# Optimization experiments

Measured on AMD Instinct MI355X. Metric: run time of the kernel, lower is better.

## Reference

```python
import jax, jax.numpy as jnp
import numpy as np

B, D, L = 2, 1024, 4096   # batch, channels (= num_heads), seq len
FS = 4                    # filter_size
DEPTH = 11                # ceil(log2((L-1)/(FS-1)+1))
LN_EPS = 1e-5


def setup_inputs() -> dict:
    key = jax.random.key(0)
    ks = jax.random.split(key, 7)
    return {
        "x": jax.random.normal(ks[0], (B, D, L), jnp.float32),
        "h0": jax.random.normal(ks[1], (D, 1, FS), jnp.float32) * 0.2,
        "h1": jax.random.normal(ks[2], (D, 1, FS), jnp.float32) * 0.2,
        "w_mix": jax.random.normal(ks[3], (D, D), jnp.float32) / np.sqrt(D),
        "b_mix": jnp.zeros((D,), jnp.float32),
        "ln_gamma": jnp.ones((D,), jnp.float32),
        "ln_beta": jnp.zeros((D,), jnp.float32),
    }


def _dw_conv(a, h, dilation):
    # depthwise (groups = D) dilated conv1d, cross-correlation like torch
    return jax.lax.conv_general_dilated(
        a, h, window_strides=(1,), padding='VALID',
        rhs_dilation=(dilation,),
        dimension_numbers=('NCH', 'OIH', 'NCH'),
        feature_group_count=D)


def reference(x, h0, h1, w_mix, b_mix, ln_gamma, ln_beta):
    # --- multires conv tree ---
    a = x
    dilation = 1
    a_list, b_list = [], []
    for _ in range(DEPTH):
        pad = dilation * (FS - 1)
        ap = jnp.pad(a, ((0, 0), (0, 0), (pad, 0)))  # left causal pad
        b = _dw_conv(ap, h1, dilation)
        a = _dw_conv(ap, h0, dilation)
        a_list.append(a)
        b_list.append(b)
        dilation *= 2
    # --- gated combination across scales (deepest level first) ---
    a_rev = a_list[::-1]
    b_rev = b_list[::-1]
    y = jnp.zeros_like(x)
    gated = None
    for i in range(DEPTH):
        if i + 1 < DEPTH:
            gated = jax.nn.sigmoid(a_rev[i]) * b_rev[i + 1]
        # last iteration reuses the previous gated tensor (matches original)
        y = y + gated
    # --- 1x1 channel mix (Dropout1d is identity in eval) + residual ---
    mixed = jnp.einsum('oc,bcl->bol', w_mix, y) + b_mix[None, :, None]
    z = mixed + x
    # --- LayerNorm over channel dim ---
    mu = jnp.mean(z, axis=1, keepdims=True)
    var = jnp.mean(jnp.square(z - mu), axis=1, keepdims=True)
    out = (z - mu) * jax.lax.rsqrt(var + LN_EPS)
    out = out * ln_gamma[None, :, None] + ln_beta[None, :, None]
    return out
```

## Files before the change

### kernel.cpp

```cpp
#include <hip/hip_runtime.h>
#include <hip/hip_bf16.h>

#define NB 2
#define ND 1024
#define NL 4096
#define NFS 4
#define NDEPTH 11
#define LN_EPS 1e-5f

#define BM 128
#define BN 128
#define BK 32

#define CPAD 384

typedef __bf16 bf16x8 __attribute__((ext_vector_type(8)));
typedef float f32x4 __attribute__((ext_vector_type(4)));

__device__ __forceinline__ unsigned short f2bf(float f) {
    __hip_bfloat16 h = __float2bfloat16(f);
    unsigned short u;
    __builtin_memcpy(&u, &h, 2);
    return u;
}

__device__ __forceinline__ float bf2f(unsigned short u) {
    unsigned int ui = (unsigned int)u << 16;
    float f;
    __builtin_memcpy(&f, &ui, 4);
    return f;
}

__device__ __forceinline__ unsigned int pack2bf(float lo, float hi) {
    return (unsigned int)f2bf(lo) | ((unsigned int)f2bf(hi) << 16);
}

__device__ __forceinline__ float sigm(float v) {
    return __builtin_amdgcn_rcpf(1.f + __expf(-v));
}

__device__ __forceinline__ void llds16(const void* g, void* l) {
    __builtin_amdgcn_global_load_lds(
        (const __attribute__((address_space(1))) unsigned int*)g,
        (__attribute__((address_space(3))) unsigned int*)l, 16, 0, 0);
}

__global__ __launch_bounds__(256) void wconv_kernel(const float* __restrict__ w,
                                                    unsigned short* __restrict__ wbf) {
    const int idx8 = (blockIdx.x * 256 + threadIdx.x) * 8;
    const float4 v0 = *reinterpret_cast<const float4*>(w + idx8);
    const float4 v1 = *reinterpret_cast<const float4*>(w + idx8 + 4);
    uint4 o;
    o.x = pack2bf(v0.x, v0.y);
    o.y = pack2bf(v0.z, v0.w);
    o.z = pack2bf(v1.x, v1.y);
    o.w = pack2bf(v1.z, v1.w);
    *reinterpret_cast<uint4*>(wbf + idx8) = o;
}

__global__ __launch_bounds__(256) void conv_cascade_kernel(const float* __restrict__ x,
                                                           const float* __restrict__ h0,
                                                           const float* __restrict__ h1,
                                                           unsigned short* __restrict__ ybf) {
    __shared__ float a_sh[CPAD + NL];
    const int row = blockIdx.x;
    const int d = row & (ND - 1);
    const int t = threadIdx.x;

    if (t < CPAD - 256) a_sh[t] = 0.f;
    a_sh[(CPAD - 256) + t] = 0.f;

    const float* xrow = x + (size_t)row * NL;

    float h0c[NFS], h1c[NFS];
#pragma unroll
    for (int k = 0; k < NFS; ++k) {
        h0c[k] = h0[d * NFS + k];
        h1c[k] = h1[d * NFS + k];
    }

    float cur[16], yacc[16], bprev[16];
#pragma unroll
    for (int i = 0; i < 16; ++i) {
        cur[i] = xrow[i * 256 + t];
        a_sh[CPAD + i * 256 + t] = cur[i];
        yacc[i] = 0.f;
        bprev[i] = 0.f;
    }
    __syncthreads();

    int dil = 1;
#pragma unroll 1
    for (int lev = 0; lev < 7; ++lev) {
        const int off1 = CPAD + t - dil;
        const int off2 = CPAD + t - 2 * dil;
        const int off3 = CPAD + t - 3 * dil;
        float anew[16], bnew[16];
#pragma unroll
        for (int i = 0; i < 16; ++i) {
            const float a0 = cur[i];
            const float a1 = a_sh[off1 + i * 256];
            const float a2 = a_sh[off2 + i * 256];
            const float a3 = a_sh[off3 + i * 256];
            anew[i] = h0c[3] * a0 + h0c[2] * a1 + h0c[1] * a2 + h0c[0] * a3;
            bnew[i] = h1c[3] * a0 + h1c[2] * a1 + h1c[1] * a2 + h1c[0] * a3;
        }
        __syncthreads();
#pragma unroll
        for (int i = 0; i < 16; ++i) a_sh[CPAD + i * 256 + t] = anew[i];

        if (lev >= 1) {
            const float sc = (lev == 1) ? 2.f : 1.f;
#pragma unroll
            for (int i = 0; i < 16; ++i)
                yacc[i] += sc * sigm(anew[i]) * bprev[i];
        }
#pragma unroll
        for (int i = 0; i < 16; ++i) {
            cur[i] = anew[i];
            bprev[i] = bnew[i];
        }
        dil <<= 1;
        __syncthreads();
    }

    {
        const int off1 = CPAD + t - 128;
        const int off2 = CPAD + t - 256;
        const int off3 = CPAD + t - 384;
        float anew[16], bnew[16];
#pragma unroll
        for (int i = 0; i < 16; ++i) {
            const float a0 = cur[i];
            const float a1 = a_sh[off1 + i * 256];
            const float a2 = a_sh[off2 + i * 256];
            const float a3 = a_sh[off3 + i * 256];
            anew[i] = h0c[3] * a0 + h0c[2] * a1 + h0c[1] * a2 + h0c[0] * a3;
            bnew[i] = h1c[3] * a0 + h1c[2] * a1 + h1c[1] * a2 + h1c[0] * a3;
        }
#pragma unroll
        for (int i = 0; i < 16; ++i) {
            yacc[i] += sigm(anew[i]) * bprev[i];
            cur[i] = anew[i];
            bprev[i] = bnew[i];
        }
    }

    {
        float anew[16], bnew[16];
#pragma unroll
        for (int i = 0; i < 16; ++i) {
            const float a0 = cur[i];
            const float a1 = (i >= 1) ? cur[i - 1] : 0.f;
            const float a2 = (i >= 2) ? cur[i - 2] : 0.f;
            const float a3 = (i >= 3) ? cur[i - 3] : 0.f;
            anew[i] = h0c[3] * a0 + h0c[2] * a1 + h0c[1] * a2 + h0c[0] * a3;
            bnew[i] = h1c[3] * a0 + h1c[2] * a1 + h1c[1] * a2 + h1c[0] * a3;
        }
#pragma unroll
        for (int i = 0; i < 16; ++i) {
            yacc[i] += sigm(anew[i]) * bprev[i];
            cur[i] = anew[i];
            bprev[i] = bnew[i];
        }
    }

    {
        float anew[16], bnew[16];
#pragma unroll
        for (int i = 0; i < 16; ++i) {
            const float a0 = cur[i];
            const float a1 = (i >= 2) ? cur[i - 2] : 0.f;
            const float a2 = (i >= 4) ? cur[i - 4] : 0.f;
            const float a3 = (i >= 6) ? cur[i - 6] : 0.f;
            anew[i] = h0c[3] * a0 + h0c[2] * a1 + h0c[1] * a2 + h0c[0] * a3;
            bnew[i] = h1c[3] * a0 + h1c[2] * a1 + h1c[1] * a2 + h1c[0] * a3;
        }
#pragma unroll
        for (int i = 0; i < 16; ++i) {
            yacc[i] += sigm(anew[i]) * bprev[i];
            cur[i] = anew[i];
            bprev[i] = bnew[i];
        }
    }

#pragma unroll
    for (int i = 0; i < 16; ++i) {
        const float a0 = cur[i];
        const float a1 = (i >= 4) ? cur[i - 4] : 0.f;
        const float a2 = (i >= 8) ? cur[i - 8] : 0.f;
        const float a3 = (i >= 12) ? cur[i - 12] : 0.f;
        const float an = h0c[3] * a0 + h0c[2] * a1 + h0c[1] * a2 + h0c[0] * a3;
        yacc[i] += sigm(an) * bprev[i];
    }

#pragma unroll
    for (int i = 0; i < 16; ++i)
        ybf[(size_t)row * NL + i * 256 + t] = f2bf(yacc[i]);
}

__global__ __launch_bounds__(256) void transpose_kernel(const unsigned short* __restrict__ ybf,
                                                        unsigned short* __restrict__ yT) {
    __shared__ unsigned short tile[64][66];
    const int l0 = blockIdx.x * 64;
    const int c0 = blockIdx.y * 64;
    const int b = blockIdx.z;
    const int t = threadIdx.x;
    const int li = t & 63, cg = t >> 6;
#pragma unroll
    for (int k = 0; k < 16; ++k) {
        const int ci = cg * 16 + k;
        tile[ci][li] = ybf[(size_t)(b * ND + c0 + ci) * NL + l0 + li];
    }
    __syncthreads();
    const int ci2 = t & 63, lg = t >> 6;
#pragma unroll
    for (int k = 0; k < 16; ++k) {
        const int li2 = lg * 16 + k;
        yT[((size_t)b * NL + l0 + li2) * ND + c0 + ci2] = tile[ci2][li2];
    }
}

__global__ __launch_bounds__(256) void gemm_kernel(const unsigned short* __restrict__ wbf,
                                                   const unsigned short* __restrict__ yT,
                                                   const float* __restrict__ bmix,
                                                   unsigned short* __restrict__ mixed) {
    __shared__ unsigned short As[BM][BK];
    __shared__ unsigned short Bs[BN][BK];

    const int n0 = blockIdx.x * BN;
    const int m0 = blockIdx.y * BM;
    const int b = blockIdx.z;
    const int t = threadIdx.x;
    const int lane = t & 63, wid = t >> 6;
    const int wr = wid >> 1, wc = wid & 1;
    const int fr = lane & 15;
    const int fk = (lane >> 4) * 8;

    const int srow = wid * 32 + (lane >> 2);
    const int sk = (lane & 3) * 8;
    const unsigned short* Ag = wbf + (size_t)(m0 + srow) * ND + sk;
    const unsigned short* Bg = yT + ((size_t)b * NL + n0 + srow) * ND + sk;
    unsigned short* AsD0 = &As[wid * 32][0];
    unsigned short* AsD1 = &As[wid * 32 + 16][0];
    unsigned short* BsD0 = &Bs[wid * 32][0];
    unsigned short* BsD1 = &Bs[wid * 32 + 16][0];

    f32x4 acc[4][4];
#pragma unroll
    for (int mi = 0; mi < 4; ++mi)
#pragma unroll
        for (int ni = 0; ni < 4; ++ni)
            acc[mi][ni] = (f32x4){0.f, 0.f, 0.f, 0.f};

    for (int kt = 0; kt < ND; kt += BK) {
        llds16(Ag + kt, AsD0);
        llds16(Ag + kt + 16 * ND, AsD1);
        llds16(Bg + kt, BsD0);
        llds16(Bg + kt + 16 * ND, BsD1);
        __syncthreads();

        bf16x8 af[4], bv[4];
#pragma unroll
        for (int mi = 0; mi < 4; ++mi)
            af[mi] = *reinterpret_cast<const bf16x8*>(&As[wr * 64 + mi * 16 + fr][fk]);
#pragma unroll
        for (int ni = 0; ni < 4; ++ni)
            bv[ni] = *reinterpret_cast<const bf16x8*>(&Bs[wc * 64 + ni * 16 + fr][fk]);
#pragma unroll
        for (int mi = 0; mi < 4; ++mi)
#pragma unroll
            for (int ni = 0; ni < 4; ++ni)
                acc[mi][ni] = __builtin_amdgcn_mfma_f32_16x16x32_bf16(af[mi], bv[ni],
                                                                      acc[mi][ni], 0, 0, 0);
        __syncthreads();
    }

    const size_t bbase = (size_t)b * ND * NL;
#pragma unroll
    for (int mi = 0; mi < 4; ++mi) {
#pragma unroll
        for (int r = 0; r < 4; ++r) {
            const int o = m0 + wr * 64 + mi * 16 + (lane >> 4) * 4 + r;
            const float bm = bmix[o];
            const size_t rowbase = bbase + (size_t)o * NL;
#pragma unroll
            for (int ni = 0; ni < 4; ++ni) {
                const int l = n0 + wc * 64 + ni * 16 + fr;
                mixed[rowbase + l] = f2bf(acc[mi][ni][r] + bm);
            }
        }
    }
}

__global__ __launch_bounds__(512) void ln_kernel(const unsigned short* __restrict__ mixed,
                                                 const float* __restrict__ x,
                                                 const float* __restrict__ gamma,
                                                 const float* __restrict__ beta,
                                                 float* __restrict__ out) {
    const int b = blockIdx.y;
    const int l0 = blockIdx.x * 32;
    const int tl = threadIdx.x & 31, tg = threadIdx.x >> 5;
    const size_t base = (size_t)b * ND * NL + l0 + tl;

    float zv[64];
    float s = 0.f, q = 0.f;
#pragma unroll
    for (int j = 0; j < 64; ++j) {
        const size_t idx = base + (size_t)(tg + j * 16) * NL;
        const float v = bf2f(mixed[idx]) + x[idx];
        zv[j] = v;
        s += v;
        q += v * v;
    }

    __shared__ float sred[16][33], qred[16][33];
    __shared__ float mu_s[32], rs_s[32];
    sred[tg][tl] = s;
    qred[tg][tl] = q;
    __syncthreads();
    if (tg == 0) {
        float S = 0.f, Q = 0.f;
#pragma unroll
        for (int g = 0; g < 16; ++g) {
            S += sred[g][tl];
            Q += qred[g][tl];
        }
        const float mu = S * (1.f / ND);
        const float var = Q * (1.f / ND) - mu * mu;
        mu_s[tl] = mu;
        rs_s[tl] = rsqrtf(var + LN_EPS);
    }
    __syncthreads();
    const float mu = mu_s[tl], rs = rs_s[tl];
#pragma unroll
    for (int j = 0; j < 64; ++j) {
        const int c = tg + j * 16;
        out[base + (size_t)c * NL] = (zv[j] - mu) * rs * gamma[c] + beta[c];
    }
}

extern "C" void kernel_launch(void* const* d_in, const int* in_sizes, int n_in,
                              void* d_out, int out_size, void* d_ws, size_t ws_size,
                              hipStream_t stream) {
    (void)in_sizes; (void)n_in; (void)out_size; (void)ws_size;
    const float* x = (const float*)d_in[0];
    const float* h0 = (const float*)d_in[1];
    const float* h1 = (const float*)d_in[2];
    const float* wmix = (const float*)d_in[3];
    const float* bmix = (const float*)d_in[4];
    const float* gamma = (const float*)d_in[5];
    const float* beta = (const float*)d_in[6];
    float* out = (float*)d_out;

    char* ws = (char*)d_ws;
    unsigned short* ybf = (unsigned short*)(ws);
    unsigned short* yT = (unsigned short*)(ws + (size_t)16 * 1024 * 1024);
    unsigned short* wbf = (unsigned short*)(ws + (size_t)32 * 1024 * 1024);
    unsigned short* mixed = (unsigned short*)(ws + (size_t)34 * 1024 * 1024);

    wconv_kernel<<<dim3(ND * ND / (256 * 8)), 256, 0, stream>>>(wmix, wbf);
    conv_cascade_kernel<<<dim3(NB * ND), 256, 0, stream>>>(x, h0, h1, ybf);
    transpose_kernel<<<dim3(NL / 64, ND / 64, NB), 256, 0, stream>>>(ybf, yT);
    gemm_kernel<<<dim3(NL / BN, ND / BM, NB), 256, 0, stream>>>(wbf, yT, bmix, mixed);
    ln_kernel<<<dim3(NL / 32, NB), 512, 0, stream>>>(mixed, x, gamma, beta, out);
}
```

Before: 108.8 us.

## Double-buffer LDS in GEMM and conv cascade to overlap loads and drop barriers

```diff
diff --git a/kernel.cpp b/kernel.cpp
--- a/kernel.cpp
+++ b/kernel.cpp
@@ -11,8 +11,10 @@
 #define BM 128
 #define BN 128
 #define BK 32
+#define NKI (ND / BK)
 
 #define CPAD 384
+#define CBUF (CPAD + NL)
 
 typedef __bf16 bf16x8 __attribute__((ext_vector_type(8)));
 typedef float f32x4 __attribute__((ext_vector_type(4)));
@@ -62,13 +64,16 @@
                                                            const float* __restrict__ h0,
                                                            const float* __restrict__ h1,
                                                            unsigned short* __restrict__ ybf) {
-    __shared__ float a_sh[CPAD + NL];
+    __shared__ float a_sh[2 * CBUF];
     const int row = blockIdx.x;
     const int d = row & (ND - 1);
     const int t = threadIdx.x;
 
-    if (t < CPAD - 256) a_sh[t] = 0.f;
-    a_sh[(CPAD - 256) + t] = 0.f;
+#pragma unroll
+    for (int j = 0; j < 2; ++j) {
+        a_sh[j * CBUF + t] = 0.f;
+        if (t < CPAD - 256) a_sh[j * CBUF + 256 + t] = 0.f;
+    }
 
     const float* xrow = x + (size_t)row * NL;
 
@@ -89,12 +94,13 @@
     }
     __syncthreads();
 
+    int rb = 0, wb = CBUF;
     int dil = 1;
 #pragma unroll 1
     for (int lev = 0; lev < 7; ++lev) {
-        const int off1 = CPAD + t - dil;
-        const int off2 = CPAD + t - 2 * dil;
-        const int off3 = CPAD + t - 3 * dil;
+        const int off1 = rb + CPAD + t - dil;
+        const int off2 = rb + CPAD + t - 2 * dil;
+        const int off3 = rb + CPAD + t - 3 * dil;
         float anew[16], bnew[16];
 #pragma unroll
         for (int i = 0; i < 16; ++i) {
@@ -105,9 +111,8 @@
             anew[i] = h0c[3] * a0 + h0c[2] * a1 + h0c[1] * a2 + h0c[0] * a3;
             bnew[i] = h1c[3] * a0 + h1c[2] * a1 + h1c[1] * a2 + h1c[0] * a3;
         }
-        __syncthreads();
-#pragma unroll
-        for (int i = 0; i < 16; ++i) a_sh[CPAD + i * 256 + t] = anew[i];
+#pragma unroll
+        for (int i = 0; i < 16; ++i) a_sh[wb + CPAD + i * 256 + t] = anew[i];
 
         if (lev >= 1) {
             const float sc = (lev == 1) ? 2.f : 1.f;
@@ -121,13 +126,14 @@
             bprev[i] = bnew[i];
         }
         dil <<= 1;
+        const int tmp = rb; rb = wb; wb = tmp;
         __syncthreads();
     }
 
     {
-        const int off1 = CPAD + t - 128;
-        const int off2 = CPAD + t - 256;
-        const int off3 = CPAD + t - 384;
+        const int off1 = rb + CPAD + t - 128;
+        const int off2 = rb + CPAD + t - 256;
+        const int off3 = rb + CPAD + t - 384;
         float anew[16], bnew[16];
 #pragma unroll
         for (int i = 0; i < 16; ++i) {
@@ -225,8 +231,8 @@
                                                    const unsigned short* __restrict__ yT,
                                                    const float* __restrict__ bmix,
                                                    unsigned short* __restrict__ mixed) {
-    __shared__ unsigned short As[BM][BK];
-    __shared__ unsigned short Bs[BN][BK];
+    __shared__ unsigned short As[2][BM][BK];
+    __shared__ unsigned short Bs[2][BN][BK];
 
     const int n0 = blockIdx.x * BN;
     const int m0 = blockIdx.y * BM;
@@ -241,10 +247,10 @@
     const int sk = (lane & 3) * 8;
     const unsigned short* Ag = wbf + (size_t)(m0 + srow) * ND + sk;
     const unsigned short* Bg = yT + ((size_t)b * NL + n0 + srow) * ND + sk;
-    unsigned short* AsD0 = &As[wid * 32][0];
-    unsigned short* AsD1 = &As[wid * 32 + 16][0];
-    unsigned short* BsD0 = &Bs[wid * 32][0];
-    unsigned short* BsD1 = &Bs[wid * 32 + 16][0];
+    unsigned short* AsD0[2] = {&As[0][wid * 32][0], &As[1][wid * 32][0]};
+    unsigned short* AsD1[2] = {&As[0][wid * 32 + 16][0], &As[1][wid * 32 + 16][0]};
+    unsigned short* BsD0[2] = {&Bs[0][wid * 32][0], &Bs[1][wid * 32][0]};
+    unsigned short* BsD1[2] = {&Bs[0][wid * 32 + 16][0], &Bs[1][wid * 32 + 16][0]};
 
     f32x4 acc[4][4];
 #pragma unroll
@@ -253,27 +259,41 @@
         for (int ni = 0; ni < 4; ++ni)
             acc[mi][ni] = (f32x4){0.f, 0.f, 0.f, 0.f};
 
-    for (int kt = 0; kt < ND; kt += BK) {
-        llds16(Ag + kt, AsD0);
-        llds16(Ag + kt + 16 * ND, AsD1);
-        llds16(Bg + kt, BsD0);
-        llds16(Bg + kt + 16 * ND, BsD1);
-        __syncthreads();
+    llds16(Ag, AsD0[0]);
+    llds16(Ag + 16 * ND, AsD1[0]);
+    llds16(Bg, BsD0[0]);
+    llds16(Bg + 16 * ND, BsD1[0]);
+    asm volatile("s_waitcnt vmcnt(0)" ::: "memory");
+    __builtin_amdgcn_s_barrier();
+
+    int cur = 0;
+#pragma unroll 1
+    for (int ki = 0; ki < NKI; ++ki) {
+        if (ki + 1 < NKI) {
+            const int kt = (ki + 1) * BK;
+            llds16(Ag + kt, AsD0[cur ^ 1]);
+            llds16(Ag + kt + 16 * ND, AsD1[cur ^ 1]);
+            llds16(Bg + kt, BsD0[cur ^ 1]);
+            llds16(Bg + kt + 16 * ND, BsD1[cur ^ 1]);
+        }
 
         bf16x8 af[4], bv[4];
 #pragma unroll
         for (int mi = 0; mi < 4; ++mi)
-            af[mi] = *reinterpret_cast<const bf16x8*>(&As[wr * 64 + mi * 16 + fr][fk]);
+            af[mi] = *reinterpret_cast<const bf16x8*>(&As[cur][wr * 64 + mi * 16 + fr][fk]);
 #pragma unroll
         for (int ni = 0; ni < 4; ++ni)
-            bv[ni] = *reinterpret_cast<const bf16x8*>(&Bs[wc * 64 + ni * 16 + fr][fk]);
+            bv[ni] = *reinterpret_cast<const bf16x8*>(&Bs[cur][wc * 64 + ni * 16 + fr][fk]);
 #pragma unroll
         for (int mi = 0; mi < 4; ++mi)
 #pragma unroll
             for (int ni = 0; ni < 4; ++ni)
                 acc[mi][ni] = __builtin_amdgcn_mfma_f32_16x16x32_bf16(af[mi], bv[ni],
                                                                       acc[mi][ni], 0, 0, 0);
-        __syncthreads();
+
+        asm volatile("s_waitcnt vmcnt(0)" ::: "memory");
+        __builtin_amdgcn_s_barrier();
+        cur ^= 1;
     }
 
     const size_t bbase = (size_t)b * ND * NL;
```

After: 108.7 us. No clear change (-0.1%).
